# Kernel tuning notes

Measured on AMD Instinct MI355X. Metric: run time of the kernel, lower is better.

The kernel has to match this reference:

```python
import jax, jax.numpy as jnp
from jax import lax
import numpy as np

OUT_SCALE = 0.001
DN = ('NCHW', 'OIHW', 'NCHW')


def _dw_res_gelu(v, w, b):
    # depthwise 3x3 conv (groups = C) + bias, residual add, exact GELU (torch nn.GELU default)
    y = lax.conv_general_dilated(v, w, (1, 1), ((1, 1), (1, 1)),
                                 feature_group_count=v.shape[1],
                                 dimension_numbers=DN)
    y = y + b[None, :, None, None]
    return jax.nn.gelu(v + y, approximate=False)


def setup_inputs() -> dict:
    key = jax.random.key(0)
    ks = jax.random.split(key, 6)
    B, C = 64, 64
    return {
        'z': jax.random.normal(ks[0], (B, C, 16, 16), jnp.float32),
        'x': jax.random.normal(ks[1], (B, C, 96, 96), jnp.float32),
        'wz': jax.random.normal(ks[2], (C, 1, 3, 3), jnp.float32) * 0.1,
        'bz': jax.random.normal(ks[3], (C,), jnp.float32) * 0.1,
        'wx': jax.random.normal(ks[4], (C, 1, 3, 3), jnp.float32) * 0.1,
        'bx': jax.random.normal(ks[5], (C,), jnp.float32) * 0.1,
    }


def reference(z, x, wz, bz, wx, bx):
    x = _dw_res_gelu(x, wx, bx)
    z = _dw_res_gelu(z, wz, bz)
    B, C, zh, zw = z.shape
    nx, _, h, w = x.shape
    # fast batched cross-correlation: view search as one image with B*C channels,
    # use templates z as [O=B, I=C, zh, zw] filters with feature_group_count=B
    xr = x.reshape(1, nx * C, h, w)
    out = lax.conv_general_dilated(xr, z, (1, 1),
                                   ((zh // 2, zh // 2), (zw // 2, zw // 2)),
                                   feature_group_count=B,
                                   dimension_numbers=DN)
    out = out.reshape(nx, -1, out.shape[-2], out.shape[-1])
    return out * OUT_SCALE
```

## Files before the change

### kernel.cpp

```cpp
#include <hip/hip_runtime.h>
#include <hip/hip_bf16.h>

typedef unsigned short ushortT;
typedef __bf16 bf16x8 __attribute__((ext_vector_type(8)));
typedef float f32x4 __attribute__((ext_vector_type(4)));

#define OUT_SCALE 0.001f

__device__ __forceinline__ float gelu_fast(float v) {
    const float u = v * fmaf(0.044715f * v, v, 1.0f);
    const float e = __expf(-1.5957691216057308f * u);
    return v * __builtin_amdgcn_rcpf(1.0f + e);
}
__device__ __forceinline__ ushortT f2bf(float f) {
    __hip_bfloat16 h = __float2bfloat16(f);
    return *reinterpret_cast<ushortT*>(&h);
}

__global__ __launch_bounds__(256) void k_gelu_z(
    const float* __restrict__ z, const float* __restrict__ wz,
    const float* __restrict__ bz, ushortT* __restrict__ zbuf)
{
    const int b   = blockIdx.x;
    const int tid = threadIdx.x;
    const int c   = tid >> 2;
    const int q   = tid & 3;

    __shared__ float   zs[64 * 260];
    __shared__ ushortT zt[16384];

    {
        const float4* src = (const float4*)(z + ((size_t)b * 64 + c) * 256 + q * 64);
        float4* dstv = (float4*)(zs + c * 260 + q * 64);
        #pragma unroll
        for (int i = 0; i < 16; ++i) dstv[i] = src[i];
    }
    __syncthreads();

    const float* wp = wz + c * 9;
    float w[9];
    #pragma unroll
    for (int i = 0; i < 9; ++i) w[i] = wp[i];
    const float bias = bz[c];
    const float* zc = zs + c * 260;

    for (int v = q * 4; v < q * 4 + 4; ++v) {
        #pragma unroll
        for (int u = 0; u < 16; ++u) {
            float acc = bias;
            #pragma unroll
            for (int dr = 0; dr < 3; ++dr) {
                const int uu = u + dr - 1;
                if (uu < 0 || uu >= 16) continue;
                #pragma unroll
                for (int dc = 0; dc < 3; ++dc) {
                    const int vv = v + dc - 1;
                    if (vv < 0 || vv >= 16) continue;
                    acc += zc[uu * 16 + vv] * w[dr * 3 + dc];
                }
            }
            const float y = acc + zc[u * 16 + v];
            zt[(v * 16 + u) * 64 + c] = f2bf(gelu_fast(y));
        }
    }
    __syncthreads();
    uint4* dst = (uint4*)(zbuf + (size_t)b * 16384);
    const uint4* s4 = (const uint4*)zt;
    for (int i = tid; i < 2048; i += 256) dst[i] = s4[i];
}

__global__ __launch_bounds__(512, 4) void k_fused(
    const float* __restrict__ x, const float* __restrict__ wx,
    const float* __restrict__ bx, const ushortT* __restrict__ zbuf,
    float* __restrict__ part)
{
    const int lin = blockIdx.x;
    const int sw  = ((lin & 7) * 192) + (lin >> 3);
    const int k   = sw % 24;
    const int b   = sw / 24;
    const int r0  = k * 4;
    const int tid = threadIdx.x;

    __shared__ ushortT rowbuf[2][8192];
    __shared__ float   outacc[19 * 113];

    for (int i = tid; i < 19 * 113; i += 512) outacc[i] = 0.f;

    {
        const int rrg = tid >> 7, t = tid & 127;
        const int off = (t < 32) ? t * 8 : 3328 + (t - 32) * 8;
        *(uint4*)(&rowbuf[0][0] + rrg * 4096 + off) = make_uint4(0, 0, 0, 0);
    }

    const int c = tid >> 3, colg = tid & 7, j0 = colg * 12;
    const int wave = tid >> 6;
    const int lane = tid & 63;
    const int n    = lane & 15;
    const int q    = lane >> 4;
    const int j0a  = wave * 16;

    float w[9];
    #pragma unroll
    for (int i = 0; i < 9; ++i) w[i] = wx[c * 9 + i];
    const float bias = bx[c];
    const float* xb = x + (size_t)(b * 64 + c) * 9216;
    const ushortT* zb = zbuf + (size_t)b * 16384;

    const int g_  = c >> 5, cl = c & 31, chunk = cl >> 3, pos = cl & 7;

    #pragma unroll
    for (int sp = 0; sp < 2; ++sp) {
        #pragma unroll
        for (int rloc = 0; rloc < 2; ++rloc) {
            const int r = r0 + sp * 2 + rloc;
            float acc[12], winc[12];
            #pragma unroll
            for (int jj = 0; jj < 12; ++jj) acc[jj] = bias;
            #pragma unroll
            for (int dr = 0; dr < 3; ++dr) {
                const int rr = r + dr - 1;
                const bool rok = (rr >= 0) && (rr < 96);
                float f[20];
                #pragma unroll
                for (int m = 0; m < 5; ++m) {
                    const int cs = j0 - 4 + 4 * m;
                    float4 v = make_float4(0.f, 0.f, 0.f, 0.f);
                    if (rok && cs >= 0 && cs <= 92)
                        v = *(const float4*)(xb + rr * 96 + cs);
                    f[4 * m] = v.x; f[4 * m + 1] = v.y;
                    f[4 * m + 2] = v.z; f[4 * m + 3] = v.w;
                }
                #pragma unroll
                for (int jj = 0; jj < 12; ++jj)
                    acc[jj] += f[jj + 3] * w[dr * 3] + f[jj + 4] * w[dr * 3 + 1]
                             + f[jj + 5] * w[dr * 3 + 2];
                if (dr == 1) {
                    #pragma unroll
                    for (int jj = 0; jj < 12; ++jj) winc[jj] = f[jj + 4];
                }
            }
            ushortT* rbw = &rowbuf[rloc][0] + g_ * 4096;
            #pragma unroll
            for (int jj = 0; jj < 12; ++jj) {
                const float gv = gelu_fast(acc[jj] + winc[jj]);
                const int T = j0 + jj + 8;
                const int schunk = chunk ^ ((T >> 1) & 3);
                rbw[T * 32 + schunk * 8 + pos] = f2bf(gv);
            }
        }
        __syncthreads();

        if (wave < 7) {
            f32x4 acc0 = {0.f, 0.f, 0.f, 0.f};
            f32x4 acc1 = {0.f, 0.f, 0.f, 0.f};
            #pragma unroll
            for (int g = 0; g < 2; ++g) {
                bf16x8 bfrag[16];
                #pragma unroll
                for (int v = 0; v < 16; ++v)
                    bfrag[v] = *(const bf16x8*)(zb + (v * 16 + n) * 64 + g * 32 + 8 * q);
                #pragma unroll
                for (int v = 0; v < 16; ++v) {
                    const int T = j0a + n + v;
                    const int off = (g * 128 + T) * 32 + ((q ^ ((T >> 1) & 3)) << 3);
                    const bf16x8 a0 = *(const bf16x8*)(&rowbuf[0][0] + off);
                    acc0 = __builtin_amdgcn_mfma_f32_16x16x32_bf16(a0, bfrag[v], acc0, 0, 0, 0);
                    const bf16x8 a1 = *(const bf16x8*)(&rowbuf[1][0] + off);
                    acc1 = __builtin_amdgcn_mfma_f32_16x16x32_bf16(a1, bfrag[v], acc1, 0, 0, 0);
                }
            }
            const int iib = sp * 2 + 15 - n;
            float* orow0 = outacc + iib * 113 + j0a + 4 * q;
            float* orow1 = outacc + (iib + 1) * 113 + j0a + 4 * q;
            #pragma unroll
            for (int g3 = 0; g3 < 4; ++g3) orow0[g3] += acc0[g3];
            #pragma unroll
            for (int g3 = 0; g3 < 4; ++g3) orow1[g3] += acc1[g3];
        }
        __syncthreads();
    }

    float* pb = part + (size_t)(b * 24 + k) * (19 * 97);
    for (int i = tid; i < 19 * 97; i += 512) {
        const int ii = i / 97, j = i - ii * 97;
        pb[i] = outacc[ii * 113 + j] * OUT_SCALE;
    }
}

__global__ __launch_bounds__(256) void k_reduce(
    const float* __restrict__ part, float* __restrict__ out)
{
    const int gid = blockIdx.x * 256 + threadIdx.x;
    if (gid >= 64 * 9409) return;
    const int b   = gid / 9409;
    const int rem = gid - b * 9409;
    const int i   = rem / 97;
    const int j   = rem - i * 97;

    const int klo = (i >= 11) ? ((i - 8) >> 2) : 0;
    int khi = (i + 7) >> 2;
    if (khi > 23) khi = 23;

    float s = 0.f;
    const float* pb = part + (size_t)b * 24 * 19 * 97;
    for (int k = klo; k <= khi; ++k) {
        const int ib = i - 4 * k + 7;
        s += pb[(k * 19 + ib) * 97 + j];
    }
    out[(size_t)b * 9409 + rem] = s;
}

extern "C" void kernel_launch(void* const* d_in, const int* in_sizes, int n_in,
                              void* d_out, int out_size, void* d_ws, size_t ws_size,
                              hipStream_t stream)
{
    const float* z  = (const float*)d_in[0];
    const float* x  = (const float*)d_in[1];
    const float* wz = (const float*)d_in[2];
    const float* bz = (const float*)d_in[3];
    const float* wx = (const float*)d_in[4];
    const float* bx = (const float*)d_in[5];
    float* out = (float*)d_out;

    ushortT* zbuf = (ushortT*)d_ws;
    float*   partw = (float*)((char*)d_ws + (size_t)64 * 16384 * 2);

    k_gelu_z<<<dim3(64), 256, 0, stream>>>(z, wz, bz, zbuf);
    k_fused<<<dim3(1536), 512, 0, stream>>>(x, wx, bx, zbuf, partw);
    const int nout = 64 * 9409;
    k_reduce<<<dim3((nout + 255) / 256), 256, 0, stream>>>(partw, out);

    (void)in_sizes; (void)n_in; (void)ws_size; (void)out_size;
}
```

Measured before the change: 348.6 us.

## Split fused kernel to two rows per block and write per-row partials directly

The fused conv+correlation kernel now handles two search rows per block instead of four, doubling the grid. Each row's MFMA result goes straight to a per-row global partial buffer, which removes the shared-memory output accumulator, its zeroing and one barrier. The reduce kernel now sums up to 16 per-row partials per output instead of about 4 per-block partials, and applies the output scale there. The z preprocessing kernel is split across four channel groups and writes bf16 straight to global memory. Trade-off: each block reloads the full z fragment set for half the work, and the partial buffer is much larger, so the reduce pass reads more data.

```diff
diff --git a/kernel.cpp b/kernel.cpp
--- a/kernel.cpp
+++ b/kernel.cpp
@@ -21,52 +21,47 @@
     const float* __restrict__ z, const float* __restrict__ wz,
     const float* __restrict__ bz, ushortT* __restrict__ zbuf)
 {
-    const int b   = blockIdx.x;
+    const int b  = blockIdx.x;
+    const int cg = blockIdx.y;
     const int tid = threadIdx.x;
-    const int c   = tid >> 2;
-    const int q   = tid & 3;
-
-    __shared__ float   zs[64 * 260];
-    __shared__ ushortT zt[16384];
-
-    {
-        const float4* src = (const float4*)(z + ((size_t)b * 64 + c) * 256 + q * 64);
-        float4* dstv = (float4*)(zs + c * 260 + q * 64);
-        #pragma unroll
-        for (int i = 0; i < 16; ++i) dstv[i] = src[i];
+
+    __shared__ float zs[16 * 260];
+
+    for (int i = tid; i < 1024; i += 256) {
+        const int c_l = i >> 6, pos = i & 63;
+        *(float4*)(zs + c_l * 260 + pos * 4) =
+            *(const float4*)(z + ((size_t)(b * 64 + cg * 16 + c_l)) * 256 + pos * 4);
     }
     __syncthreads();
 
-    const float* wp = wz + c * 9;
+    const int c_l = tid & 15;
+    const int v   = tid >> 4;
+    const int c   = cg * 16 + c_l;
+
     float w[9];
     #pragma unroll
-    for (int i = 0; i < 9; ++i) w[i] = wp[i];
+    for (int i = 0; i < 9; ++i) w[i] = wz[c * 9 + i];
     const float bias = bz[c];
-    const float* zc = zs + c * 260;
-
-    for (int v = q * 4; v < q * 4 + 4; ++v) {
-        #pragma unroll
-        for (int u = 0; u < 16; ++u) {
-            float acc = bias;
-            #pragma unroll
-            for (int dr = 0; dr < 3; ++dr) {
-                const int uu = u + dr - 1;
-                if (uu < 0 || uu >= 16) continue;
-                #pragma unroll
-                for (int dc = 0; dc < 3; ++dc) {
-                    const int vv = v + dc - 1;
-                    if (vv < 0 || vv >= 16) continue;
-                    acc += zc[uu * 16 + vv] * w[dr * 3 + dc];
-                }
-            }
-            const float y = acc + zc[u * 16 + v];
-            zt[(v * 16 + u) * 64 + c] = f2bf(gelu_fast(y));
-        }
-    }
-    __syncthreads();
-    uint4* dst = (uint4*)(zbuf + (size_t)b * 16384);
-    const uint4* s4 = (const uint4*)zt;
-    for (int i = tid; i < 2048; i += 256) dst[i] = s4[i];
+    const float* zc = zs + c_l * 260;
+    ushortT* zo = zbuf + (size_t)b * 16384 + c;
+
+    #pragma unroll
+    for (int u = 0; u < 16; ++u) {
+        float acc = bias;
+        #pragma unroll
+        for (int dr = 0; dr < 3; ++dr) {
+            const int uu = u + dr - 1;
+            if (uu < 0 || uu >= 16) continue;
+            #pragma unroll
+            for (int dc = 0; dc < 3; ++dc) {
+                const int vv = v + dc - 1;
+                if (vv < 0 || vv >= 16) continue;
+                acc += zc[uu * 16 + vv] * w[dr * 3 + dc];
+            }
+        }
+        const float y = acc + zc[u * 16 + v];
+        zo[(v * 16 + u) * 64] = f2bf(gelu_fast(y));
+    }
 }
 
 __global__ __launch_bounds__(512, 4) void k_fused(
@@ -75,115 +70,102 @@
     float* __restrict__ part)
 {
     const int lin = blockIdx.x;
-    const int sw  = ((lin & 7) * 192) + (lin >> 3);
-    const int k   = sw % 24;
-    const int b   = sw / 24;
-    const int r0  = k * 4;
+    const int sw  = ((lin & 7) * 384) + (lin >> 3);
+    const int k2  = sw % 48;
+    const int b   = sw / 48;
+    const int r0  = k2 * 2;
     const int tid = threadIdx.x;
 
     __shared__ ushortT rowbuf[2][8192];
-    __shared__ float   outacc[19 * 113];
-
-    for (int i = tid; i < 19 * 113; i += 512) outacc[i] = 0.f;
 
     {
-        const int rrg = tid >> 7, t = tid & 127;
+        const int row = tid >> 8, g = (tid >> 7) & 1, t = tid & 127;
         const int off = (t < 32) ? t * 8 : 3328 + (t - 32) * 8;
-        *(uint4*)(&rowbuf[0][0] + rrg * 4096 + off) = make_uint4(0, 0, 0, 0);
+        *(uint4*)(&rowbuf[row][g * 4096 + off]) = make_uint4(0, 0, 0, 0);
     }
 
     const int c = tid >> 3, colg = tid & 7, j0 = colg * 12;
+    const int g_ = c >> 5, cl = c & 31, chunk = cl >> 3, pos = cl & 7;
+
+    float w[9];
+    #pragma unroll
+    for (int i = 0; i < 9; ++i) w[i] = wx[c * 9 + i];
+    const float bias = bx[c];
+    const float* xb = x + (size_t)(b * 64 + c) * 9216;
+
+    #pragma unroll
+    for (int rloc = 0; rloc < 2; ++rloc) {
+        const int r = r0 + rloc;
+        float acc[12], winc[12];
+        #pragma unroll
+        for (int jj = 0; jj < 12; ++jj) acc[jj] = bias;
+        #pragma unroll
+        for (int dr = 0; dr < 3; ++dr) {
+            const int rr = r + dr - 1;
+            const bool rok = (rr >= 0) && (rr < 96);
+            float f[20];
+            #pragma unroll
+            for (int m = 0; m < 5; ++m) {
+                const int cs = j0 - 4 + 4 * m;
+                float4 v = make_float4(0.f, 0.f, 0.f, 0.f);
+                if (rok && cs >= 0 && cs <= 92)
+                    v = *(const float4*)(xb + rr * 96 + cs);
+                f[4 * m] = v.x; f[4 * m + 1] = v.y;
+                f[4 * m + 2] = v.z; f[4 * m + 3] = v.w;
+            }
+            #pragma unroll
+            for (int jj = 0; jj < 12; ++jj)
+                acc[jj] += f[jj + 3] * w[dr * 3] + f[jj + 4] * w[dr * 3 + 1]
+                         + f[jj + 5] * w[dr * 3 + 2];
+            if (dr == 1) {
+                #pragma unroll
+                for (int jj = 0; jj < 12; ++jj) winc[jj] = f[jj + 4];
+            }
+        }
+        ushortT* rbw = &rowbuf[rloc][0] + g_ * 4096;
+        #pragma unroll
+        for (int jj = 0; jj < 12; ++jj) {
+            const float gv = gelu_fast(acc[jj] + winc[jj]);
+            const int T = j0 + jj + 8;
+            const int schunk = chunk ^ ((T >> 1) & 3);
+            rbw[T * 32 + schunk * 8 + pos] = f2bf(gv);
+        }
+    }
+    __syncthreads();
+
     const int wave = tid >> 6;
     const int lane = tid & 63;
     const int n    = lane & 15;
     const int q    = lane >> 4;
-    const int j0a  = wave * 16;
-
-    float w[9];
-    #pragma unroll
-    for (int i = 0; i < 9; ++i) w[i] = wx[c * 9 + i];
-    const float bias = bx[c];
-    const float* xb = x + (size_t)(b * 64 + c) * 9216;
-    const ushortT* zb = zbuf + (size_t)b * 16384;
-
-    const int g_  = c >> 5, cl = c & 31, chunk = cl >> 3, pos = cl & 7;
-
-    #pragma unroll
-    for (int sp = 0; sp < 2; ++sp) {
-        #pragma unroll
-        for (int rloc = 0; rloc < 2; ++rloc) {
-            const int r = r0 + sp * 2 + rloc;
-            float acc[12], winc[12];
-            #pragma unroll
-            for (int jj = 0; jj < 12; ++jj) acc[jj] = bias;
-            #pragma unroll
-            for (int dr = 0; dr < 3; ++dr) {
-                const int rr = r + dr - 1;
-                const bool rok = (rr >= 0) && (rr < 96);
-                float f[20];
-                #pragma unroll
-                for (int m = 0; m < 5; ++m) {
-                    const int cs = j0 - 4 + 4 * m;
-                    float4 v = make_float4(0.f, 0.f, 0.f, 0.f);
-                    if (rok && cs >= 0 && cs <= 92)
-                        v = *(const float4*)(xb + rr * 96 + cs);
-                    f[4 * m] = v.x; f[4 * m + 1] = v.y;
-                    f[4 * m + 2] = v.z; f[4 * m + 3] = v.w;
-                }
-                #pragma unroll
-                for (int jj = 0; jj < 12; ++jj)
-                    acc[jj] += f[jj + 3] * w[dr * 3] + f[jj + 4] * w[dr * 3 + 1]
-                             + f[jj + 5] * w[dr * 3 + 2];
-                if (dr == 1) {
-                    #pragma unroll
-                    for (int jj = 0; jj < 12; ++jj) winc[jj] = f[jj + 4];
-                }
-            }
-            ushortT* rbw = &rowbuf[rloc][0] + g_ * 4096;
-            #pragma unroll
-            for (int jj = 0; jj < 12; ++jj) {
-                const float gv = gelu_fast(acc[jj] + winc[jj]);
-                const int T = j0 + jj + 8;
-                const int schunk = chunk ^ ((T >> 1) & 3);
-                rbw[T * 32 + schunk * 8 + pos] = f2bf(gv);
-            }
-        }
-        __syncthreads();
-
-        if (wave < 7) {
-            f32x4 acc0 = {0.f, 0.f, 0.f, 0.f};
-            f32x4 acc1 = {0.f, 0.f, 0.f, 0.f};
-            #pragma unroll
-            for (int g = 0; g < 2; ++g) {
-                bf16x8 bfrag[16];
-                #pragma unroll
-                for (int v = 0; v < 16; ++v)
-                    bfrag[v] = *(const bf16x8*)(zb + (v * 16 + n) * 64 + g * 32 + 8 * q);
-                #pragma unroll
-                for (int v = 0; v < 16; ++v) {
-                    const int T = j0a + n + v;
-                    const int off = (g * 128 + T) * 32 + ((q ^ ((T >> 1) & 3)) << 3);
-                    const bf16x8 a0 = *(const bf16x8*)(&rowbuf[0][0] + off);
-                    acc0 = __builtin_amdgcn_mfma_f32_16x16x32_bf16(a0, bfrag[v], acc0, 0, 0, 0);
-                    const bf16x8 a1 = *(const bf16x8*)(&rowbuf[1][0] + off);
-                    acc1 = __builtin_amdgcn_mfma_f32_16x16x32_bf16(a1, bfrag[v], acc1, 0, 0, 0);
-                }
-            }
-            const int iib = sp * 2 + 15 - n;
-            float* orow0 = outacc + iib * 113 + j0a + 4 * q;
-            float* orow1 = outacc + (iib + 1) * 113 + j0a + 4 * q;
-            #pragma unroll
-            for (int g3 = 0; g3 < 4; ++g3) orow0[g3] += acc0[g3];
-            #pragma unroll
-            for (int g3 = 0; g3 < 4; ++g3) orow1[g3] += acc1[g3];
-        }
-        __syncthreads();
-    }
-
-    float* pb = part + (size_t)(b * 24 + k) * (19 * 97);
-    for (int i = tid; i < 19 * 97; i += 512) {
-        const int ii = i / 97, j = i - ii * 97;
-        pb[i] = outacc[ii * 113 + j] * OUT_SCALE;
+    if (wave < 7) {
+        const int j0a = wave * 16;
+        const ushortT* zb = zbuf + (size_t)b * 16384;
+        f32x4 acc0 = {0.f, 0.f, 0.f, 0.f};
+        f32x4 acc1 = {0.f, 0.f, 0.f, 0.f};
+
+        #pragma unroll
+        for (int g = 0; g < 2; ++g) {
+            bf16x8 bfrag[16];
+            #pragma unroll
+            for (int v = 0; v < 16; ++v)
+                bfrag[v] = *(const bf16x8*)(zb + (v * 16 + n) * 64 + g * 32 + 8 * q);
+            #pragma unroll
+            for (int v = 0; v < 16; ++v) {
+                const int T = j0a + n + v;
+                const int off = (g * 128 + T) * 32 + ((q ^ ((T >> 1) & 3)) << 3);
+                const bf16x8 a0 = *(const bf16x8*)(&rowbuf[0][0] + off);
+                acc0 = __builtin_amdgcn_mfma_f32_16x16x32_bf16(a0, bfrag[v], acc0, 0, 0, 0);
+                const bf16x8 a1 = *(const bf16x8*)(&rowbuf[1][0] + off);
+                acc1 = __builtin_amdgcn_mfma_f32_16x16x32_bf16(a1, bfrag[v], acc1, 0, 0, 0);
+            }
+        }
+
+        const int ii = 15 - n;
+        const int joff = j0a + 4 * q;
+        f32x4* p0 = (f32x4*)(part + ((size_t)(b * 96 + r0) * 16 + ii) * 112 + joff);
+        *p0 = acc0;
+        f32x4* p1 = (f32x4*)(part + ((size_t)(b * 96 + r0 + 1) * 16 + ii) * 112 + joff);
+        *p1 = acc1;
     }
 }
 
@@ -197,17 +179,16 @@
     const int i   = rem / 97;
     const int j   = rem - i * 97;
 
-    const int klo = (i >= 11) ? ((i - 8) >> 2) : 0;
-    int khi = (i + 7) >> 2;
-    if (khi > 23) khi = 23;
-
+    int rlo = i - 8;  if (rlo < 0)  rlo = 0;
+    int rhi = i + 7;  if (rhi > 95) rhi = 95;
+
+    const float* p = part + ((size_t)(b * 96 + rlo) * 16 + (i - rlo + 7)) * 112 + j;
     float s = 0.f;
-    const float* pb = part + (size_t)b * 24 * 19 * 97;
-    for (int k = klo; k <= khi; ++k) {
-        const int ib = i - 4 * k + 7;
-        s += pb[(k * 19 + ib) * 97 + j];
-    }
-    out[(size_t)b * 9409 + rem] = s;
+    for (int r = rlo; r <= rhi; ++r) {
+        s += *p;
+        p += 1680;
+    }
+    out[(size_t)b * 9409 + rem] = s * OUT_SCALE;
 }
 
 extern "C" void kernel_launch(void* const* d_in, const int* in_sizes, int n_in,
@@ -225,8 +206,8 @@
     ushortT* zbuf = (ushortT*)d_ws;
     float*   partw = (float*)((char*)d_ws + (size_t)64 * 16384 * 2);
 
-    k_gelu_z<<<dim3(64), 256, 0, stream>>>(z, wz, bz, zbuf);
-    k_fused<<<dim3(1536), 512, 0, stream>>>(x, wx, bx, zbuf, partw);
+    k_gelu_z<<<dim3(64, 4), 256, 0, stream>>>(z, wz, bz, zbuf);
+    k_fused<<<dim3(3072), 512, 0, stream>>>(x, wx, bx, zbuf, partw);
     const int nout = 64 * 9409;
     k_reduce<<<dim3((nout + 255) / 256), 256, 0, stream>>>(partw, out);
 
```

Result: faster. 332.0 us (-4.8%).
